# Optimization experiments

Hardware: AMD Instinct MI355X
Metric: run time of the kernel (lower is better)

Reference implementation:

```python
import jax, jax.numpy as jnp
import numpy as np

jax.config.update("jax_enable_x64", True)  # original uses double for Cholesky stability

LAM = 1.0


def _safe_pow(x, a):
    # |x|**a, with a gradient-safe handling of x == 0 (result is 0 for a > 0;
    # naive 0**a has nan grad w.r.t. a via log(0)).
    ax = jnp.abs(x)
    safe = jnp.where(ax == 0, 1.0, ax)
    return jnp.where(ax == 0, 0.0, safe ** a)


def _dx_cov(alpha, tau, T):
    # fGn (increment) covariance; stationary -> depends only on lag k = j - i (Toeplitz)
    t = jnp.arange(T - 1, dtype=jnp.float64)
    DT = (t[None, :] - t[:, None])[None, :, :]          # [1, T-1, T-1]
    a = alpha[:, None, None].astype(jnp.float64)        # [BS, 1, 1]
    tb = tau[:, None, None].astype(jnp.float64)
    R = 0.5 * (_safe_pow(DT + 1.0, a) + _safe_pow(DT - 1.0, a) - 2.0 * _safe_pow(DT, a))
    adt = jnp.abs(DT)
    # exponential taper beyond lag tau; clamp exponent so unused branch can't overflow
    decay = jnp.exp(-LAM * jnp.maximum(adt - tb, 0.0))
    R = jnp.where(adt >= tb, R * decay, R)
    return R                                            # [BS, T-1, T-1] float64


def setup_inputs() -> dict:
    key = jax.random.key(0)
    k1, k2, k3, k4 = jax.random.split(key, 4)
    BS, T, dim = 64, 1024, 3
    alpha = (0.5 + jax.random.uniform(k1, (BS,))).astype(jnp.float32)        # (0.5, 1.5) valid fBM exponent
    tau = (20.0 + 50.0 * jax.random.uniform(k2, (BS,))).astype(jnp.float32)  # taper lag > 0
    diffusion = (0.5 + jax.random.uniform(k3, (BS,))).astype(jnp.float32)
    du = jax.random.normal(k4, (BS, T - 1, dim), dtype=jnp.float32)          # hoisted torch.randn
    return {"alpha": alpha, "tau": tau, "diffusion": diffusion, "du": du, "T": T}


def reference(alpha, tau, diffusion, du, T):
    BS, dim = alpha.shape[0], du.shape[-1]
    C = _dx_cov(alpha, tau, T)                           # [BS, T-1, T-1] float64
    L = jnp.linalg.cholesky(C).astype(jnp.float32)       # batched Cholesky, cast like torch
    du_s = du * jnp.sqrt(diffusion)[:, None, None]       # scale noise by sqrt(D)
    dx = L @ du_s                                        # [BS, T-1, dim]
    x = jnp.cumsum(dx, axis=1)
    zeros = jnp.zeros((BS, 1, dim), dtype=x.dtype)
    return jnp.concatenate([zeros, x], axis=1)           # [BS, T, dim]
```

## Files before the change

kernel.cpp:

```cpp
#include <hip/hip_runtime.h>
#include <math.h>


#define TM1 1023
#define NTH 1024
#define K0  128
#define CSTRIDE 129

__device__ __forceinline__ float bperm(int a, float v) {
    return __int_as_float(__builtin_amdgcn_ds_bpermute(a, __float_as_int(v)));
}
__device__ __forceinline__ float rdlane(float v, int s) {
    return __int_as_float(__builtin_amdgcn_readlane(__float_as_int(v), s));
}
__device__ __forceinline__ float dpp_shl1(float v) {
    return __int_as_float(__builtin_amdgcn_update_dpp(
        0, __float_as_int(v), 0x130, 0xF, 0xF, true));
}
template<int CTRL, int RM, bool BC>
__device__ __forceinline__ float dppadd(float s) {
    float t = __int_as_float(__builtin_amdgcn_update_dpp(
        0, __float_as_int(s), CTRL, RM, 0xF, BC));
    return s + t;
}
__device__ __forceinline__ float dpp_scan(float s) {
    s = dppadd<0x111, 0xF, true >(s);
    s = dppadd<0x112, 0xF, true >(s);
    s = dppadd<0x114, 0xF, true >(s);
    s = dppadd<0x118, 0xF, true >(s);
    s = dppadd<0x142, 0xA, false>(s);
    s = dppadd<0x143, 0xC, false>(s);
    return s;
}
__device__ __forceinline__ int uslot(int k) { return ((k & 3) << 8) | (k >> 2); }

__device__ __forceinline__ float4 ldus(const float4* us4s, int k) {
    int kc = (k < 0) ? 0 : k;
    float4 v = us4s[uslot(kc)];
    if (k < 0) { v.x = 0.f; v.y = 0.f; v.z = 0.f; }
    return v;
}

template<bool MIXED>
__device__ __forceinline__ void conv_quad(
    const float4* us4s, const float* colDT, float lca, float lcb,
    int B, int jq, int quad, int K, float4* ypx4, float4* ypy4, float4* ypz4)
{
    const int      j0   = jq << 5;
    const float    lsel = (jq < 2) ? lca : lcb;
    const unsigned Ku   = (unsigned)K;

    float4 q0 = MIXED ? ldus(us4s, B + 0 - j0) : us4s[uslot(B + 0 - j0)];
    float4 q1 = MIXED ? ldus(us4s, B + 1 - j0) : us4s[uslot(B + 1 - j0)];
    float4 q2 = MIXED ? ldus(us4s, B + 2 - j0) : us4s[uslot(B + 2 - j0)];
    float4 q3 = MIXED ? ldus(us4s, B + 3 - j0) : us4s[uslot(B + 3 - j0)];

    float a0x=0,a0y=0,a0z=0, a1x=0,a1y=0,a1z=0;
    float a2x=0,a2y=0,a2z=0, a3x=0,a3y=0,a3z=0;

    #pragma unroll 8
    for (int jj = 0; jj < 32; ++jj) {
        const int j = j0 + jj;
        float lcj = rdlane(lsel, j & 63);
        float c0 = lcj, c1 = lcj, c2 = lcj, c3 = lcj;
        if (MIXED) {
            int p = B - j;
            float4 h = *reinterpret_cast<const float4*>(&colDT[(j << 7) + B]);
            c0 = ((unsigned)(p + 0) < Ku) ? h.x : lcj;
            c1 = ((unsigned)(p + 1) < Ku) ? h.y : lcj;
            c2 = ((unsigned)(p + 2) < Ku) ? h.z : lcj;
            c3 = ((unsigned)(p + 3) < Ku) ? h.w : lcj;
        }
        a0x = fmaf(c0, q0.x, a0x); a0y = fmaf(c0, q0.y, a0y); a0z = fmaf(c0, q0.z, a0z);
        a1x = fmaf(c1, q1.x, a1x); a1y = fmaf(c1, q1.y, a1y); a1z = fmaf(c1, q1.z, a1z);
        a2x = fmaf(c2, q2.x, a2x); a2y = fmaf(c2, q2.y, a2y); a2z = fmaf(c2, q2.z, a2z);
        a3x = fmaf(c3, q3.x, a3x); a3y = fmaf(c3, q3.y, a3y); a3z = fmaf(c3, q3.z, a3z);
        int xi = B - j - 1;
        float4 nv = MIXED ? ldus(us4s, xi) : us4s[uslot(xi)];
        q3 = q2; q2 = q1; q1 = q0; q0 = nv;
    }
    ypx4[(jq << 8) + quad] = make_float4(a0x, a1x, a2x, a3x);
    ypy4[(jq << 8) + quad] = make_float4(a0y, a1y, a2y, a3y);
    ypz4[(jq << 8) + quad] = make_float4(a0z, a1z, a2z, a3z);
}

__global__ __launch_bounds__(NTH, 1)
void fbm_schur_kernel(const float* __restrict__ alpha,
                      const float* __restrict__ tau,
                      const float* __restrict__ diffusion,
                      const float* __restrict__ du,
                      float* __restrict__ out)
{
    const int b   = blockIdx.x;
    const int tid = threadIdx.x;
    const int w   = tid >> 6;
    const int l   = tid & 63;

    __shared__ float  colDT[K0 * CSTRIDE];
    __shared__ float4 us4[1024];
    __shared__ float4 ypx4[4 * 256];
    __shared__ float4 ypy4[4 * 256];
    __shared__ float4 ypz4[4 * 256];
    __shared__ float  Lc[128];
    __shared__ float  wtot[48];

    const float sd = sqrtf(diffusion[b]);
    const float tv = tau[b];
    const int   K  = min(K0, (int)ceilf(tv) + 48);
    const float* dub = du + (size_t)b * (TM1 * 3);

    if (w > 0) {
        for (int e = tid - 64; e < TM1 * 3; e += (NTH - 64)) {
            int k = e / 3, d = e - 3 * k;
            ((float*)&us4[uslot(k)])[d] = dub[e] * sd;
        }
        for (int i = tid - 64; i < K0; i += (NTH - 64))
            colDT[i * CSTRIDE + 128] = 0.f;
        if (tid == 64) us4[uslot(1023)] = make_float4(0.f, 0.f, 0.f, 0.f);
    } else {
        const double a  = (double)alpha[b];
        const double tb = (double)tv;
        double pa = pow((double)(l == 0 ? 128 : l), a);
        double pb = pow((double)(l + 64), a);
        double pam1 = __shfl_up(pa, 1);
        double pap1 = __shfl_down(pa, 1);
        double pbm1 = __shfl_up(pb, 1);
        double pbp1 = __shfl_down(pb, 1);
        double p63  = __shfl(pa, 63);
        double p64  = __shfl(pb, 0);
        double p128 = __shfl(pa, 0);
        if (l == 1)  pam1 = 0.0;
        if (l == 63) pap1 = p64;
        if (l == 0)  pbm1 = p63;
        if (l == 63) pbp1 = p128;
        auto covk = [&](int k, double pm, double p0, double pp) -> float {
            if (k == 0) return 1.0f;
            double ck = 0.5 * (pp + pm - 2.0 * p0);
            double dk = (double)k;
            if (dk >= tb) ck *= exp(tb - dk);
            return (float)ck;
        };
        float g1a = covk(l,      pam1, (l == 0 ? 0.0 : pa), pap1);
        float g1b = covk(l + 64, pbm1, pb,                  pbp1);
        float g2a = (l == 0) ? 0.f : g1a;
        float g2b = g1b;

        int probe = __builtin_amdgcn_update_dpp(0, l + 100, 0x130, 0xF, 0xF, true);
        const bool dpp_ok = (__builtin_amdgcn_readlane(probe, 5) == 106);
        const int addr_up = ((l + 1) & 63) << 2;

        float den = 1.0f, rcpden = 1.0f, sc = 1.0f;
#define SCHUR_LOOP(SHA, SHB)                                               \
        for (int k = 0; k < K; ++k) {                                      \
            colDT[l * CSTRIDE + k]        = g1a * sc;                      \
            colDT[(64 + l) * CSTRIDE + k] = g1b * sc;                      \
            float num  = rdlane(g2a, 1);                                   \
            float r    = num * rcpden;                                     \
            float wrap = rdlane(g2b, 0);                                   \
            float g2pa = (SHA);                                            \
            float g2pb = (SHB);                                            \
            if (l == 63) { g2pa = wrap; g2pb = 0.f; }                      \
            float n1a = fmaf(-r, g2pa, g1a);                               \
            float n1b = fmaf(-r, g2pb, g1b);                               \
            g2a = fmaf(-r, g1a, g2pa);                                     \
            g2b = fmaf(-r, g1b, g2pb);                                     \
            g1a = n1a; g1b = n1b;                                          \
            den    = fmaf(-r, num, den);                                   \
            rcpden = __builtin_amdgcn_rcpf(den);                           \
            sc     = __frsqrt_rn(den);                                     \
        }
        if (dpp_ok) {
            SCHUR_LOOP(dpp_shl1(g2a), dpp_shl1(g2b))
        } else {
            SCHUR_LOOP(bperm(addr_up, g2a), bperm(addr_up, g2b))
        }
#undef SCHUR_LOOP
        Lc[l]      = g1a * sc;
        Lc[64 + l] = g1b * sc;
    }
    __syncthreads();

    {
        float lca = Lc[l], lcb = Lc[64 + l];
        const int jq   = w & 3;
        const int rb   = w >> 2;
        const int quad = (rb << 6) + l;
        const int B    = quad << 2;
        if (rb == 0)
            conv_quad<true >(us4, colDT, lca, lcb, B, jq, quad, K, ypx4, ypy4, ypz4);
        else
            conv_quad<false>(us4, colDT, lca, lcb, B, jq, quad, K, ypx4, ypy4, ypz4);
    }
    __syncthreads();

    const int i = tid;
    float sx = 0.f, sy = 0.f, sz = 0.f;
    if (i < TM1) {
        const float* px = (const float*)ypx4;
        const float* py = (const float*)ypy4;
        const float* pz = (const float*)ypz4;
        sx = px[i] + px[1024 + i] + px[2048 + i] + px[3072 + i];
        sy = py[i] + py[1024 + i] + py[2048 + i] + py[3072 + i];
        sz = pz[i] + pz[1024 + i] + pz[2048 + i] + pz[3072 + i];
    }
    {
        float pv = dpp_scan(1.0f);
        const bool scan_ok = (rdlane(pv, 63) == 64.0f) && (rdlane(pv, 21) == 22.0f);
        if (scan_ok) {
            sx = dpp_scan(sx); sy = dpp_scan(sy); sz = dpp_scan(sz);
        } else {
            #pragma unroll
            for (int off = 1; off < 64; off <<= 1) {
                float tx = __shfl_up(sx, off);
                float ty = __shfl_up(sy, off);
                float tz = __shfl_up(sz, off);
                if (l >= off) { sx += tx; sy += ty; sz += tz; }
            }
        }
    }
    if (l == 63) { wtot[w * 3 + 0] = sx; wtot[w * 3 + 1] = sy; wtot[w * 3 + 2] = sz; }
    __syncthreads();

    float ox = 0.f, oy = 0.f, oz = 0.f;
    for (int q = 0; q < w; ++q) {
        ox += wtot[q * 3 + 0]; oy += wtot[q * 3 + 1]; oz += wtot[q * 3 + 2];
    }
    float* outb = out + (size_t)b * (TM1 + 1) * 3;
    if (i < TM1) {
        outb[(i + 1) * 3 + 0] = sx + ox;
        outb[(i + 1) * 3 + 1] = sy + oy;
        outb[(i + 1) * 3 + 2] = sz + oz;
    }
    if (tid == 0) { outb[0] = 0.f; outb[1] = 0.f; outb[2] = 0.f; }
}

extern "C" void kernel_launch(void* const* d_in, const int* in_sizes, int n_in,
                              void* d_out, int out_size, void* d_ws, size_t ws_size,
                              hipStream_t stream)
{
    const float* alpha     = (const float*)d_in[0];
    const float* tau       = (const float*)d_in[1];
    const float* diffusion = (const float*)d_in[2];
    const float* du        = (const float*)d_in[3];
    float* out = (float*)d_out;
    const int BS = in_sizes[0];

    fbm_schur_kernel<<<dim3(BS), dim3(NTH), 0, stream>>>(
        alpha, tau, diffusion, du, out);
}
```

Baseline: 76.39 us.

## Restructure banded convolution with register sliding windows and planar noise layout

Switches the scaled noise from an interleaved float4 slot layout to three planar arrays. The banded convolution is rewritten so waves 0-3 each compute 12 output rows per lane for the steady-state region from a register sliding window, and waves 12-15 handle the first 256 mixed rows that use colDT. The j-loop is also trimmed to K instead of always 32 steps per quarter. This aims to cut LDS loads per FMA and skip work beyond the taper length K. In exchange, waves 4-11 now sit idle during the convolution, register pressure rises, and a second DPP shift encoding is probed.

Result: no change. 77.17 us (+1.0%).

```diff
diff --git a/kernel.cpp b/kernel.cpp
--- a/kernel.cpp
+++ b/kernel.cpp
@@ -6,6 +6,7 @@
 #define NTH 1024
 #define K0  128
 #define CSTRIDE 129
+#define USN 1024
 
 __device__ __forceinline__ float bperm(int a, float v) {
     return __int_as_float(__builtin_amdgcn_ds_bpermute(a, __float_as_int(v)));
@@ -13,9 +14,10 @@
 __device__ __forceinline__ float rdlane(float v, int s) {
     return __int_as_float(__builtin_amdgcn_readlane(__float_as_int(v), s));
 }
-__device__ __forceinline__ float dpp_shl1(float v) {
+template<int CTRL>
+__device__ __forceinline__ float dppmov(float v) {
     return __int_as_float(__builtin_amdgcn_update_dpp(
-        0, __float_as_int(v), 0x130, 0xF, 0xF, true));
+        0, __float_as_int(v), CTRL, 0xF, 0xF, true));
 }
 template<int CTRL, int RM, bool BC>
 __device__ __forceinline__ float dppadd(float s) {
@@ -31,57 +33,6 @@
     s = dppadd<0x142, 0xA, false>(s);
     s = dppadd<0x143, 0xC, false>(s);
     return s;
-}
-__device__ __forceinline__ int uslot(int k) { return ((k & 3) << 8) | (k >> 2); }
-
-__device__ __forceinline__ float4 ldus(const float4* us4s, int k) {
-    int kc = (k < 0) ? 0 : k;
-    float4 v = us4s[uslot(kc)];
-    if (k < 0) { v.x = 0.f; v.y = 0.f; v.z = 0.f; }
-    return v;
-}
-
-template<bool MIXED>
-__device__ __forceinline__ void conv_quad(
-    const float4* us4s, const float* colDT, float lca, float lcb,
-    int B, int jq, int quad, int K, float4* ypx4, float4* ypy4, float4* ypz4)
-{
-    const int      j0   = jq << 5;
-    const float    lsel = (jq < 2) ? lca : lcb;
-    const unsigned Ku   = (unsigned)K;
-
-    float4 q0 = MIXED ? ldus(us4s, B + 0 - j0) : us4s[uslot(B + 0 - j0)];
-    float4 q1 = MIXED ? ldus(us4s, B + 1 - j0) : us4s[uslot(B + 1 - j0)];
-    float4 q2 = MIXED ? ldus(us4s, B + 2 - j0) : us4s[uslot(B + 2 - j0)];
-    float4 q3 = MIXED ? ldus(us4s, B + 3 - j0) : us4s[uslot(B + 3 - j0)];
-
-    float a0x=0,a0y=0,a0z=0, a1x=0,a1y=0,a1z=0;
-    float a2x=0,a2y=0,a2z=0, a3x=0,a3y=0,a3z=0;
-
-    #pragma unroll 8
-    for (int jj = 0; jj < 32; ++jj) {
-        const int j = j0 + jj;
-        float lcj = rdlane(lsel, j & 63);
-        float c0 = lcj, c1 = lcj, c2 = lcj, c3 = lcj;
-        if (MIXED) {
-            int p = B - j;
-            float4 h = *reinterpret_cast<const float4*>(&colDT[(j << 7) + B]);
-            c0 = ((unsigned)(p + 0) < Ku) ? h.x : lcj;
-            c1 = ((unsigned)(p + 1) < Ku) ? h.y : lcj;
-            c2 = ((unsigned)(p + 2) < Ku) ? h.z : lcj;
-            c3 = ((unsigned)(p + 3) < Ku) ? h.w : lcj;
-        }
-        a0x = fmaf(c0, q0.x, a0x); a0y = fmaf(c0, q0.y, a0y); a0z = fmaf(c0, q0.z, a0z);
-        a1x = fmaf(c1, q1.x, a1x); a1y = fmaf(c1, q1.y, a1y); a1z = fmaf(c1, q1.z, a1z);
-        a2x = fmaf(c2, q2.x, a2x); a2y = fmaf(c2, q2.y, a2y); a2z = fmaf(c2, q2.z, a2z);
-        a3x = fmaf(c3, q3.x, a3x); a3y = fmaf(c3, q3.y, a3y); a3z = fmaf(c3, q3.z, a3z);
-        int xi = B - j - 1;
-        float4 nv = MIXED ? ldus(us4s, xi) : us4s[uslot(xi)];
-        q3 = q2; q2 = q1; q1 = q0; q0 = nv;
-    }
-    ypx4[(jq << 8) + quad] = make_float4(a0x, a1x, a2x, a3x);
-    ypy4[(jq << 8) + quad] = make_float4(a0y, a1y, a2y, a3y);
-    ypz4[(jq << 8) + quad] = make_float4(a0z, a1z, a2z, a3z);
 }
 
 __global__ __launch_bounds__(NTH, 1)
@@ -96,13 +47,11 @@
     const int w   = tid >> 6;
     const int l   = tid & 63;
 
-    __shared__ float  colDT[K0 * CSTRIDE];
-    __shared__ float4 us4[1024];
-    __shared__ float4 ypx4[4 * 256];
-    __shared__ float4 ypy4[4 * 256];
-    __shared__ float4 ypz4[4 * 256];
-    __shared__ float  Lc[128];
-    __shared__ float  wtot[48];
+    __shared__ float colDT[K0 * CSTRIDE];
+    __shared__ float usx[USN], usy[USN], usz[USN];
+    __shared__ float plx[4][1024], ply[4][1024], plz[4][1024];
+    __shared__ float LcS[128];
+    __shared__ float wtot[48];
 
     const float sd = sqrtf(diffusion[b]);
     const float tv = tau[b];
@@ -111,12 +60,12 @@
 
     if (w > 0) {
         for (int e = tid - 64; e < TM1 * 3; e += (NTH - 64)) {
-            int k = e / 3, d = e - 3 * k;
-            ((float*)&us4[uslot(k)])[d] = dub[e] * sd;
-        }
-        for (int i = tid - 64; i < K0; i += (NTH - 64))
-            colDT[i * CSTRIDE + 128] = 0.f;
-        if (tid == 64) us4[uslot(1023)] = make_float4(0.f, 0.f, 0.f, 0.f);
+            int t = e / 3, d = e - 3 * t;
+            float v = dub[e] * sd;
+            float* dst = (d == 0) ? usx : (d == 1) ? usy : usz;
+            dst[t] = v;
+        }
+        if (tid == 64) { usx[1023] = 0.f; usy[1023] = 0.f; usz[1023] = 0.f; }
     } else {
         const double a  = (double)alpha[b];
         const double tb = (double)tv;
@@ -145,8 +94,10 @@
         float g2a = (l == 0) ? 0.f : g1a;
         float g2b = g1b;
 
-        int probe = __builtin_amdgcn_update_dpp(0, l + 100, 0x130, 0xF, 0xF, true);
-        const bool dpp_ok = (__builtin_amdgcn_readlane(probe, 5) == 106);
+        int p130 = __builtin_amdgcn_update_dpp(0, l + 100, 0x130, 0xF, 0xF, true);
+        const bool ok130 = (__builtin_amdgcn_readlane(p130, 5) == 106);
+        int p138 = __builtin_amdgcn_update_dpp(0, l + 100, 0x138, 0xF, 0xF, true);
+        const bool ok138 = (__builtin_amdgcn_readlane(p138, 5) == 106);
         const int addr_up = ((l + 1) & 63) << 2;
 
         float den = 1.0f, rcpden = 1.0f, sc = 1.0f;
@@ -169,39 +120,143 @@
             rcpden = __builtin_amdgcn_rcpf(den);                           \
             sc     = __frsqrt_rn(den);                                     \
         }
-        if (dpp_ok) {
-            SCHUR_LOOP(dpp_shl1(g2a), dpp_shl1(g2b))
-        } else {
-            SCHUR_LOOP(bperm(addr_up, g2a), bperm(addr_up, g2b))
-        }
+        if (ok130)      { SCHUR_LOOP(dppmov<0x130>(g2a), dppmov<0x130>(g2b)) }
+        else if (ok138) { SCHUR_LOOP(dppmov<0x138>(g2a), dppmov<0x138>(g2b)) }
+        else            { SCHUR_LOOP(bperm(addr_up, g2a), bperm(addr_up, g2b)) }
 #undef SCHUR_LOOP
-        Lc[l]      = g1a * sc;
-        Lc[64 + l] = g1b * sc;
+        LcS[l]      = g1a * sc;
+        LcS[64 + l] = g1b * sc;
     }
     __syncthreads();
 
-    {
-        float lca = Lc[l], lcb = Lc[64 + l];
-        const int jq   = w & 3;
-        const int rb   = w >> 2;
-        const int quad = (rb << 6) + l;
-        const int B    = quad << 2;
-        if (rb == 0)
-            conv_quad<true >(us4, colDT, lca, lcb, B, jq, quad, K, ypx4, ypy4, ypz4);
-        else
-            conv_quad<false>(us4, colDT, lca, lcb, B, jq, quad, K, ypx4, ypy4, ypz4);
+    const float lca = LcS[l], lcb = LcS[64 + l];
+
+    if (w < 4) {
+        const int jq = w, j0 = jq << 5;
+        const int B  = 256 + 12 * l;
+        const int G  = max(0, min(8, (K - j0 + 3) >> 2));
+        const float lsel = (jq < 2) ? lca : lcb;
+        const int t00 = B - j0 - 4;
+        float wx[16], wy[16], wz[16];
+        #pragma unroll
+        for (int bk = 0; bk < 4; ++bk) {
+            float4 vx = *(const float4*)&usx[t00 + 4 * bk];
+            float4 vy = *(const float4*)&usy[t00 + 4 * bk];
+            float4 vz = *(const float4*)&usz[t00 + 4 * bk];
+            wx[4*bk]=vx.x; wx[4*bk+1]=vx.y; wx[4*bk+2]=vx.z; wx[4*bk+3]=vx.w;
+            wy[4*bk]=vy.x; wy[4*bk+1]=vy.y; wy[4*bk+2]=vy.z; wy[4*bk+3]=vy.w;
+            wz[4*bk]=vz.x; wz[4*bk+1]=vz.y; wz[4*bk+2]=vz.z; wz[4*bk+3]=vz.w;
+        }
+        float ax[12], ay[12], az[12];
+        #pragma unroll
+        for (int i = 0; i < 12; ++i) { ax[i]=0.f; ay[i]=0.f; az[i]=0.f; }
+
+        #pragma unroll
+        for (int g = 0; g < 8; ++g) {
+            if (g < G) {
+                const int jg = j0 + 4 * g;
+                #pragma unroll
+                for (int s = 0; s < 4; ++s) {
+                    float lc = rdlane(lsel, (jg + s) & 63);
+                    #pragma unroll
+                    for (int i = 0; i < 12; ++i) {
+                        const int dd = ((i - s + 4 - 4 * g) + 64) & 15;
+                        ax[i] = fmaf(lc, wx[dd], ax[i]);
+                        ay[i] = fmaf(lc, wy[dd], ay[i]);
+                        az[i] = fmaf(lc, wz[dd], az[i]);
+                    }
+                }
+                {
+                    const int tnb = t00 - 4 * (g + 1);
+                    const int s0  = ((-4 * (g + 1)) + 64) & 15;
+                    float4 vx = *(const float4*)&usx[tnb];
+                    float4 vy = *(const float4*)&usy[tnb];
+                    float4 vz = *(const float4*)&usz[tnb];
+                    wx[s0]=vx.x; wx[s0+1]=vx.y; wx[s0+2]=vx.z; wx[s0+3]=vx.w;
+                    wy[s0]=vy.x; wy[s0+1]=vy.y; wy[s0+2]=vy.z; wy[s0+3]=vy.w;
+                    wz[s0]=vz.x; wz[s0+1]=vz.y; wz[s0+2]=vz.z; wz[s0+3]=vz.w;
+                }
+            }
+        }
+        #pragma unroll
+        for (int r4 = 0; r4 < 3; ++r4) {
+            *(float4*)&plx[jq][B + 4*r4] = make_float4(ax[4*r4],ax[4*r4+1],ax[4*r4+2],ax[4*r4+3]);
+            *(float4*)&ply[jq][B + 4*r4] = make_float4(ay[4*r4],ay[4*r4+1],ay[4*r4+2],ay[4*r4+3]);
+            *(float4*)&plz[jq][B + 4*r4] = make_float4(az[4*r4],az[4*r4+1],az[4*r4+2],az[4*r4+3]);
+        }
+    } else if (w >= 12) {
+        const int jq = w - 12, j0 = jq << 5;
+        const int B  = l << 2;
+        const int G  = max(0, min(8, (K - j0 + 3) >> 2));
+        const float lsel = (jq < 2) ? lca : lcb;
+        const unsigned Ku = (unsigned)K;
+        const int t00 = B - j0 - 4;
+        float wx[8], wy[8], wz[8];
+        #pragma unroll
+        for (int bk = 0; bk < 2; ++bk) {
+            const int tb = t00 + 4 * bk;
+            const int tc = max(tb, 0);
+            float4 vx = *(const float4*)&usx[tc];
+            float4 vy = *(const float4*)&usy[tc];
+            float4 vz = *(const float4*)&usz[tc];
+            const bool ok = tb >= 0;
+            wx[4*bk]=ok?vx.x:0.f; wx[4*bk+1]=ok?vx.y:0.f; wx[4*bk+2]=ok?vx.z:0.f; wx[4*bk+3]=ok?vx.w:0.f;
+            wy[4*bk]=ok?vy.x:0.f; wy[4*bk+1]=ok?vy.y:0.f; wy[4*bk+2]=ok?vy.z:0.f; wy[4*bk+3]=ok?vy.w:0.f;
+            wz[4*bk]=ok?vz.x:0.f; wz[4*bk+1]=ok?vz.y:0.f; wz[4*bk+2]=ok?vz.z:0.f; wz[4*bk+3]=ok?vz.w:0.f;
+        }
+        float ax[4], ay[4], az[4];
+        #pragma unroll
+        for (int i = 0; i < 4; ++i) { ax[i]=0.f; ay[i]=0.f; az[i]=0.f; }
+
+        #pragma unroll
+        for (int g = 0; g < 8; ++g) {
+            if (g < G) {
+                const int jg = j0 + 4 * g;
+                #pragma unroll
+                for (int s = 0; s < 4; ++s) {
+                    const int j = jg + s;
+                    float lc = rdlane(lsel, j & 63);
+                    float4 h = *(const float4*)&colDT[(j << 7) + B];
+                    const int p = B - j;
+                    float c0 = ((unsigned)(p + 0) < Ku) ? h.x : lc;
+                    float c1 = ((unsigned)(p + 1) < Ku) ? h.y : lc;
+                    float c2 = ((unsigned)(p + 2) < Ku) ? h.z : lc;
+                    float c3 = ((unsigned)(p + 3) < Ku) ? h.w : lc;
+                    const int d0 = ((0 - s + 4 - 4 * g) + 64) & 7;
+                    const int d1 = ((1 - s + 4 - 4 * g) + 64) & 7;
+                    const int d2 = ((2 - s + 4 - 4 * g) + 64) & 7;
+                    const int d3 = ((3 - s + 4 - 4 * g) + 64) & 7;
+                    ax[0]=fmaf(c0,wx[d0],ax[0]); ay[0]=fmaf(c0,wy[d0],ay[0]); az[0]=fmaf(c0,wz[d0],az[0]);
+                    ax[1]=fmaf(c1,wx[d1],ax[1]); ay[1]=fmaf(c1,wy[d1],ay[1]); az[1]=fmaf(c1,wz[d1],az[1]);
+                    ax[2]=fmaf(c2,wx[d2],ax[2]); ay[2]=fmaf(c2,wy[d2],ay[2]); az[2]=fmaf(c2,wz[d2],az[2]);
+                    ax[3]=fmaf(c3,wx[d3],ax[3]); ay[3]=fmaf(c3,wy[d3],ay[3]); az[3]=fmaf(c3,wz[d3],az[3]);
+                }
+                {
+                    const int tnb = t00 - 4 * (g + 1);
+                    const int tc  = max(tnb, 0);
+                    const int s0  = ((-4 * (g + 1)) + 64) & 7;
+                    float4 vx = *(const float4*)&usx[tc];
+                    float4 vy = *(const float4*)&usy[tc];
+                    float4 vz = *(const float4*)&usz[tc];
+                    const bool ok = tnb >= 0;
+                    wx[s0]=ok?vx.x:0.f; wx[s0+1]=ok?vx.y:0.f; wx[s0+2]=ok?vx.z:0.f; wx[s0+3]=ok?vx.w:0.f;
+                    wy[s0]=ok?vy.x:0.f; wy[s0+1]=ok?vy.y:0.f; wy[s0+2]=ok?vy.z:0.f; wy[s0+3]=ok?vy.w:0.f;
+                    wz[s0]=ok?vz.x:0.f; wz[s0+1]=ok?vz.y:0.f; wz[s0+2]=ok?vz.z:0.f; wz[s0+3]=ok?vz.w:0.f;
+                }
+            }
+        }
+        *(float4*)&plx[jq][B] = make_float4(ax[0], ax[1], ax[2], ax[3]);
+        *(float4*)&ply[jq][B] = make_float4(ay[0], ay[1], ay[2], ay[3]);
+        *(float4*)&plz[jq][B] = make_float4(az[0], az[1], az[2], az[3]);
     }
     __syncthreads();
 
     const int i = tid;
     float sx = 0.f, sy = 0.f, sz = 0.f;
     if (i < TM1) {
-        const float* px = (const float*)ypx4;
-        const float* py = (const float*)ypy4;
-        const float* pz = (const float*)ypz4;
-        sx = px[i] + px[1024 + i] + px[2048 + i] + px[3072 + i];
-        sy = py[i] + py[1024 + i] + py[2048 + i] + py[3072 + i];
-        sz = pz[i] + pz[1024 + i] + pz[2048 + i] + pz[3072 + i];
+        sx = plx[0][i] + plx[1][i] + plx[2][i] + plx[3][i];
+        sy = ply[0][i] + ply[1][i] + ply[2][i] + ply[3][i];
+        sz = plz[0][i] + plz[1][i] + plz[2][i] + plz[3][i];
     }
     {
         float pv = dpp_scan(1.0f);
```
